# Kernel tuning notes

Hardware: AMD Instinct MI355X
Metric: run time of the kernel (lower is better)

The kernel has to match this reference:

```python
import jax, jax.numpy as jnp
import numpy as np

N_USER = 100000
N_ITEM = 50000
EMB = 64
LAYERS = 3
N_INTER = 2000000
BATCH = 4096


def setup_inputs() -> dict:
    key = jax.random.key(0)
    ks = jax.random.split(key, 12)
    N = N_USER + N_ITEM
    # bipartite interactions u -> i, symmetrized
    u = jax.random.randint(ks[0], (N_INTER,), 0, N_USER, dtype=jnp.int32)
    i = jax.random.randint(ks[1], (N_INTER,), 0, N_ITEM, dtype=jnp.int32) + N_USER
    edge_src = jnp.concatenate([u, i])
    edge_dst = jnp.concatenate([i, u])
    # symmetric normalization D^-1/2 A D^-1/2 (as in getSparseGraph)
    deg = jnp.bincount(edge_dst, length=N).astype(jnp.float32)
    d_inv_sqrt = jnp.where(deg > 0, jax.lax.rsqrt(jnp.maximum(deg, 1.0)), 0.0)
    edge_w = d_inv_sqrt[edge_src] * d_inv_sqrt[edge_dst]
    s = 1.0 / np.sqrt(EMB)  # xavier-ish scale
    inp = {
        "user_emb": jax.random.normal(ks[2], (N_USER, EMB), jnp.float32) * s,
        "item_emb": jax.random.normal(ks[3], (N_ITEM, EMB), jnp.float32) * s,
        "W_gc": jax.random.normal(ks[4], (LAYERS, EMB, EMB), jnp.float32) * s,
        "b_gc": jax.random.normal(ks[5], (LAYERS, 1, EMB), jnp.float32) * s,
        "W_bi": jax.random.normal(ks[6], (LAYERS, EMB, EMB), jnp.float32) * s,
        "b_bi": jax.random.normal(ks[7], (LAYERS, 1, EMB), jnp.float32) * s,
        "edge_w": edge_w,
        "edge_src": edge_src,
        "edge_dst": edge_dst,
        "users": jax.random.randint(ks[8], (BATCH,), 0, N_USER, dtype=jnp.int64),
        "pos_items": jax.random.randint(ks[9], (BATCH,), 0, N_ITEM, dtype=jnp.int64),
        "neg_items": jax.random.randint(ks[10], (BATCH,), 0, N_ITEM, dtype=jnp.int64),
    }
    return inp


def reference(user_emb, item_emb, W_gc, b_gc, W_bi, b_bi, edge_w,
              edge_src, edge_dst, users, pos_items, neg_items):
    n_user = user_emb.shape[0]
    N = n_user + item_emb.shape[0]
    ego = jnp.concatenate([user_emb, item_emb], axis=0)  # [N, d]
    all_embeddings = [ego]
    for k in range(W_gc.shape[0]):
        # SpMM: side = A_hat @ ego  (gather + weighted scatter-add)
        side = jax.ops.segment_sum(ego[edge_src] * edge_w[:, None], edge_dst,
                                   num_segments=N)
        sum_e = side @ W_gc[k] + b_gc[k]
        bi_e = (ego * side) @ W_bi[k] + b_bi[k]
        ego = jax.nn.leaky_relu(sum_e + bi_e, negative_slope=0.2)
        # dropout omitted (eval mode / identity for deterministic baseline)
        nrm = jnp.linalg.norm(ego, axis=1, keepdims=True)
        all_embeddings.append(ego / jnp.maximum(nrm, 1e-12))
    all_e = jnp.concatenate(all_embeddings, axis=1)  # [N, (L+1)*d]
    u_g = all_e[:n_user][users]
    i_g = all_e[n_user:]
    return (u_g, i_g[pos_items], i_g[neg_items])
```

## Files before the change

### kernel.cpp

```cpp
#include <hip/hip_runtime.h>

#define EMB 64
#define B2SHIFT 8
#define B2ROWS 256
#define MAXB 1024

typedef short v8s __attribute__((ext_vector_type(8)));
typedef float v4f __attribute__((ext_vector_type(4)));

__device__ __forceinline__ float b2f(unsigned short u) {
    return __uint_as_float(((unsigned int)u) << 16);
}
__device__ __forceinline__ unsigned short f2b(float f) {
    unsigned int u = __float_as_uint(f);
    u += 0x7FFF + ((u >> 16) & 1);
    return (unsigned short)(u >> 16);
}

__global__ void k_init_ego(const float* __restrict__ user_emb,
                           const float* __restrict__ item_emb,
                           const float* __restrict__ dsq,
                           unsigned short* __restrict__ egob,
                           unsigned short* __restrict__ egow,
                           unsigned short* __restrict__ all_eb,
                           int n_user, int N) {
    int idx = blockIdx.x * blockDim.x + threadIdx.x;
    int total = N * EMB;
    if (idx >= total) return;
    int n = idx >> 6;
    int c = idx & 63;
    float v = (n < n_user) ? user_emb[idx] : item_emb[(size_t)(n - n_user) * EMB + c];
    unsigned short b = f2b(v);
    egob[idx] = b;
    egow[idx] = f2b(dsq[n] * v);
    all_eb[(size_t)n * 256 + c] = b;
}

__global__ __launch_bounds__(256) void k_bhist(const int* __restrict__ dst,
                                               int* __restrict__ bins,
                                               int M, int nb2) {
    __shared__ int h[MAXB];
    for (int i = threadIdx.x; i < nb2; i += 256) h[i] = 0;
    __syncthreads();
    for (int e = blockIdx.x * 256 + threadIdx.x; e < M; e += gridDim.x * 256)
        atomicAdd(&h[dst[e] >> B2SHIFT], 1);
    __syncthreads();
    for (int i = threadIdx.x; i < nb2; i += 256)
        if (h[i]) atomicAdd(&bins[i], h[i]);
}

__global__ __launch_bounds__(1024) void k_bscan(const int* __restrict__ bins,
                                                int* __restrict__ boff,
                                                int* __restrict__ bcur,
                                                int* __restrict__ row_ptr,
                                                int P, int N) {
    __shared__ int buf[1024];
    int tid = threadIdx.x;
    int v = (tid < P) ? bins[tid] : 0;
    buf[tid] = v;
    __syncthreads();
    for (int d = 1; d < 1024; d <<= 1) {
        int add = (tid >= d) ? buf[tid - d] : 0;
        __syncthreads();
        buf[tid] += add;
        __syncthreads();
    }
    if (tid < P) {
        int excl = buf[tid] - v;
        boff[tid] = excl;
        bcur[tid] = excl;
    }
    if (tid == P - 1) {
        boff[P] = buf[tid];
        row_ptr[N] = buf[tid];
    }
}

__global__ __launch_bounds__(256) void k_bin(const int* __restrict__ src,
                                             const int* __restrict__ dst,
                                             int* __restrict__ bcur,
                                             int* __restrict__ binned,
                                             int M, int nb2) {
    __shared__ int hist[MAXB];
    __shared__ int runcur[MAXB];
    int chunk = (M + gridDim.x - 1) / gridDim.x;
    int lo = blockIdx.x * chunk;
    int hi = min(lo + chunk, M);
    for (int i = threadIdx.x; i < nb2; i += 256) hist[i] = 0;
    __syncthreads();
    for (int e = lo + threadIdx.x; e < hi; e += 256)
        atomicAdd(&hist[dst[e] >> B2SHIFT], 1);
    __syncthreads();
    for (int i = threadIdx.x; i < nb2; i += 256) {
        int c = hist[i];
        runcur[i] = c ? atomicAdd(&bcur[i], c) : 0;
    }
    __syncthreads();
    for (int e = lo + threadIdx.x; e < hi; e += 256) {
        int d = dst[e];
        int pos = atomicAdd(&runcur[d >> B2SHIFT], 1);
        binned[pos] = (src[e] << B2SHIFT) | (d & (B2ROWS - 1));
    }
}

__global__ __launch_bounds__(256) void k_csrb(const int* __restrict__ boff,
                                              const int* __restrict__ binned,
                                              int* __restrict__ row_ptr,
                                              float* __restrict__ dsq,
                                              int* __restrict__ csr, int N) {
    __shared__ int hist[B2ROWS];
    __shared__ int scan[B2ROWS];
    int b = blockIdx.x;
    int beg = boff[b], end = boff[b + 1];
    int tid = threadIdx.x;
    hist[tid] = 0;
    __syncthreads();
    for (int e = beg + tid; e < end; e += 256)
        atomicAdd(&hist[binned[e] & (B2ROWS - 1)], 1);
    __syncthreads();
    int c = hist[tid];
    scan[tid] = c;
    __syncthreads();
    for (int d = 1; d < B2ROWS; d <<= 1) {
        int add = (tid >= d) ? scan[tid - d] : 0;
        __syncthreads();
        scan[tid] += add;
        __syncthreads();
    }
    int excl = beg + scan[tid] - c;
    int node = (b << B2SHIFT) + tid;
    if (node < N) {
        row_ptr[node] = excl;
        dsq[node] = (c > 0) ? rsqrtf((float)c) : 0.0f;
    }
    __syncthreads();
    hist[tid] = excl;
    __syncthreads();
    for (int e = beg + tid; e < end; e += 256) {
        int v = binned[e];
        int pos = atomicAdd(&hist[v & (B2ROWS - 1)], 1);
        csr[pos] = v >> B2SHIFT;
    }
}

__global__ __launch_bounds__(256) void k_side(const int* __restrict__ row_ptr,
                                              const int* __restrict__ csr,
                                              const float* __restrict__ dsq,
                                              const unsigned short* __restrict__ egow,
                                              const unsigned short* __restrict__ egob,
                                              unsigned short* __restrict__ X, int N) {
    int wave = threadIdx.x >> 6;
    int lane = threadIdx.x & 63;
    int n = blockIdx.x * 4 + wave;
    if (n >= N) return;
    int beg = __builtin_amdgcn_readfirstlane(row_ptr[n]);
    int end = __builtin_amdgcn_readfirstlane(row_ptr[n + 1]);
    float a0 = 0.f, a1 = 0.f, a2 = 0.f, a3 = 0.f;
    int e = beg;
    while (e < end) {
        int take = end - e;
        if (take > 64) take = 64;
        int vidx = csr[min(e + lane, end - 1)];
        int j = 0;
        for (; j + 8 <= take; j += 8) {
            int s0 = __builtin_amdgcn_readlane(vidx, j + 0);
            int s1 = __builtin_amdgcn_readlane(vidx, j + 1);
            int s2 = __builtin_amdgcn_readlane(vidx, j + 2);
            int s3 = __builtin_amdgcn_readlane(vidx, j + 3);
            int s4 = __builtin_amdgcn_readlane(vidx, j + 4);
            int s5 = __builtin_amdgcn_readlane(vidx, j + 5);
            int s6 = __builtin_amdgcn_readlane(vidx, j + 6);
            int s7 = __builtin_amdgcn_readlane(vidx, j + 7);
            float v0 = b2f(egow[(size_t)s0 * EMB + lane]);
            float v1 = b2f(egow[(size_t)s1 * EMB + lane]);
            float v2 = b2f(egow[(size_t)s2 * EMB + lane]);
            float v3 = b2f(egow[(size_t)s3 * EMB + lane]);
            float v4 = b2f(egow[(size_t)s4 * EMB + lane]);
            float v5 = b2f(egow[(size_t)s5 * EMB + lane]);
            float v6 = b2f(egow[(size_t)s6 * EMB + lane]);
            float v7 = b2f(egow[(size_t)s7 * EMB + lane]);
            a0 += v0 + v4;
            a1 += v1 + v5;
            a2 += v2 + v6;
            a3 += v3 + v7;
        }
        for (; j < take; j++) {
            int s = __builtin_amdgcn_readlane(vidx, j);
            a0 += b2f(egow[(size_t)s * EMB + lane]);
        }
        e += take;
    }
    float s = dsq[n] * ((a0 + a1) + (a2 + a3));
    float eg = b2f(egob[(size_t)n * EMB + lane]);
    X[(size_t)n * 128 + lane] = f2b(s);
    X[(size_t)n * 128 + 64 + lane] = f2b(s * eg);
}

__global__ __launch_bounds__(256, 2) void k_mt(
        const unsigned short* __restrict__ X,
        unsigned short* __restrict__ egob, unsigned short* __restrict__ egow,
        const float* __restrict__ dsq,
        const float* __restrict__ Wgc, const float* __restrict__ bgc,
        const float* __restrict__ Wbi, const float* __restrict__ bbi,
        unsigned short* __restrict__ all_eb, int N, int layer_col) {
    __shared__ unsigned short sWT[64 * 136];
    __shared__ float sB[64];
    int tid = threadIdx.x;
    for (int i = tid; i < 64 * 64; i += 256) {
        int k = i >> 6, n = i & 63;
        sWT[n * 136 + k]      = f2b(Wgc[i]);
        sWT[n * 136 + 64 + k] = f2b(Wbi[i]);
    }
    if (tid < 64) sB[tid] = bgc[tid] + bbi[tid];
    __syncthreads();

    int wave = tid >> 6, lane = tid & 63;
    int q = lane >> 4, col = lane & 15;

    v8s Bf[4][4];
#pragma unroll
    for (int nt = 0; nt < 4; nt++)
#pragma unroll
        for (int kt = 0; kt < 4; kt++)
            Bf[nt][kt] = *(const v8s*)&sWT[(nt * 16 + col) * 136 + kt * 32 + q * 8];

    int nrt = (N + 15) >> 4;
    int rt0 = (blockIdx.x * 4 + wave) * 4;
    int rt1 = min(rt0 + 4, nrt);
    for (int t = rt0; t < rt1; t++) {
        int r0 = t << 4;
        int rowA = min(r0 + col, N - 1);
        v8s Af[4];
#pragma unroll
        for (int kt = 0; kt < 4; kt++)
            Af[kt] = *(const v8s*)&X[(size_t)rowA * 128 + kt * 32 + q * 8];
        v4f acc[4];
#pragma unroll
        for (int nt = 0; nt < 4; nt++) {
            float b = sB[nt * 16 + col];
            acc[nt] = (v4f){b, b, b, b};
        }
#pragma unroll
        for (int kt = 0; kt < 4; kt++)
#pragma unroll
            for (int nt = 0; nt < 4; nt++)
                acc[nt] = __builtin_amdgcn_mfma_f32_16x16x32_bf16(
                    Af[kt], Bf[nt][kt], acc[nt], 0, 0, 0);
#pragma unroll
        for (int reg = 0; reg < 4; reg++) {
            int row = r0 + q * 4 + reg;
            float v[4];
            float ssq = 0.f;
#pragma unroll
            for (int nt = 0; nt < 4; nt++) {
                float x = acc[nt][reg];
                x = x > 0.f ? x : 0.2f * x;
                v[nt] = x;
                ssq += x * x;
            }
            ssq += __shfl_xor(ssq, 1, 64);
            ssq += __shfl_xor(ssq, 2, 64);
            ssq += __shfl_xor(ssq, 4, 64);
            ssq += __shfl_xor(ssq, 8, 64);
            float inv = 1.0f / fmaxf(sqrtf(ssq), 1e-12f);
            if (row < N) {
                float dn = dsq[row];
#pragma unroll
                for (int nt = 0; nt < 4; nt++) {
                    int c = nt * 16 + col;
                    egob[(size_t)row * EMB + c] = f2b(v[nt]);
                    egow[(size_t)row * EMB + c] = f2b(v[nt] * dn);
                    all_eb[(size_t)row * 256 + layer_col + c] = f2b(v[nt] * inv);
                }
            }
        }
    }
}

__global__ void k_gather(const unsigned short* __restrict__ all_eb,
                         const int* __restrict__ users,
                         const int* __restrict__ pos,
                         const int* __restrict__ neg,
                         float* __restrict__ out, int n_user, int batch) {
    int idx = blockIdx.x * blockDim.x + threadIdx.x;
    int total = batch * 256;
    if (idx >= 3 * total) return;
    int which = idx / total;
    int r = idx - which * total;
    int b = r >> 8;
    int c = r & 255;
    int node;
    if (which == 0) node = users[b];
    else if (which == 1) node = n_user + pos[b];
    else node = n_user + neg[b];
    out[idx] = b2f(all_eb[(size_t)node * 256 + c]);
}

static inline size_t align256(size_t x) { return (x + 255) & ~(size_t)255; }

extern "C" void kernel_launch(void* const* d_in, const int* in_sizes, int n_in,
                              void* d_out, int out_size, void* d_ws, size_t ws_size,
                              hipStream_t stream) {
    const float* user_emb = (const float*)d_in[0];
    const float* item_emb = (const float*)d_in[1];
    const float* W_gc = (const float*)d_in[2];
    const float* b_gc = (const float*)d_in[3];
    const float* W_bi = (const float*)d_in[4];
    const float* b_bi = (const float*)d_in[5];
    const int* edge_src = (const int*)d_in[7];
    const int* edge_dst = (const int*)d_in[8];
    const int* users = (const int*)d_in[9];
    const int* pos = (const int*)d_in[10];
    const int* neg = (const int*)d_in[11];

    int n_user = in_sizes[0] / EMB;
    int n_item = in_sizes[1] / EMB;
    int N = n_user + n_item;
    int M = in_sizes[6];
    int layers = in_sizes[2] / (EMB * EMB);
    int batch = in_sizes[9];
    float* out = (float*)d_out;

    int nb2 = (N + B2ROWS - 1) >> B2SHIFT;
    int nrt = (N + 15) >> 4;

    char* p = (char*)d_ws;
    unsigned short* egob = (unsigned short*)p;   p += align256((size_t)N * EMB * 2);
    unsigned short* egow = (unsigned short*)p;   p += align256((size_t)N * EMB * 2);
    unsigned short* X = (unsigned short*)p;      p += align256((size_t)N * 128 * 2);
    unsigned short* all_eb = (unsigned short*)p; p += align256((size_t)N * 256 * 2);
    float* dsq = (float*)p;            p += align256((size_t)N * 4);
    int* row_ptr = (int*)p;            p += align256((size_t)(N + 1) * 4);
    int* bins = (int*)p;               p += align256((size_t)nb2 * 4);
    int* boff = (int*)p;               p += align256((size_t)(nb2 + 1) * 4);
    int* bcur = (int*)p;               p += align256((size_t)nb2 * 4);
    int* binned = (int*)p;             p += align256((size_t)M * 4);
    int* csr = (int*)p;                p += align256((size_t)M * 4);

    hipMemsetAsync(bins, 0, (size_t)nb2 * 4, stream);

    k_bhist<<<512, 256, 0, stream>>>(edge_dst, bins, M, nb2);
    k_bscan<<<1, 1024, 0, stream>>>(bins, boff, bcur, row_ptr, nb2, N);
    k_bin<<<512, 256, 0, stream>>>(edge_src, edge_dst, bcur, binned, M, nb2);
    k_csrb<<<nb2, 256, 0, stream>>>(boff, binned, row_ptr, dsq, csr, N);

    k_init_ego<<<(N * EMB + 255) / 256, 256, 0, stream>>>(
        user_emb, item_emb, dsq, egob, egow, all_eb, n_user, N);

    for (int k = 0; k < layers; k++) {
        k_side<<<(N + 3) / 4, 256, 0, stream>>>(row_ptr, csr, dsq, egow, egob, X, N);
        k_mt<<<(nrt + 15) / 16, 256, 0, stream>>>(
            X, egob, egow, dsq,
            W_gc + (size_t)k * EMB * EMB, b_gc + (size_t)k * EMB,
            W_bi + (size_t)k * EMB * EMB, b_bi + (size_t)k * EMB,
            all_eb, N, (k + 1) * EMB);
    }

    k_gather<<<(3 * batch * 256 + 255) / 256, 256, 0, stream>>>(
        all_eb, users, pos, neg, out, n_user, batch);
}
```

Measured before the change: 622.3 us.

## Fuse ego init into CSR build, unroll gather by 16, nontemporal all_eb stores

Folds the initial embedding conversion (bf16 ego, degree-scaled ego, layer-0 output) into the per-bin CSR build kernel, so one launch and the re-read of dsq go away. Adds a 16-wide unrolled neighbour gather loop in the SpMM kernel to keep more loads in flight. Writes to the concatenated output buffer use nontemporal stores so they pollute the cache less. The unrolled loop raises register pressure, and the fused kernel does serial work inside 586 blocks, which may lower parallelism for the init step.

```diff
diff --git a/kernel.cpp b/kernel.cpp
--- a/kernel.cpp
+++ b/kernel.cpp
@@ -15,25 +15,6 @@
     unsigned int u = __float_as_uint(f);
     u += 0x7FFF + ((u >> 16) & 1);
     return (unsigned short)(u >> 16);
-}
-
-__global__ void k_init_ego(const float* __restrict__ user_emb,
-                           const float* __restrict__ item_emb,
-                           const float* __restrict__ dsq,
-                           unsigned short* __restrict__ egob,
-                           unsigned short* __restrict__ egow,
-                           unsigned short* __restrict__ all_eb,
-                           int n_user, int N) {
-    int idx = blockIdx.x * blockDim.x + threadIdx.x;
-    int total = N * EMB;
-    if (idx >= total) return;
-    int n = idx >> 6;
-    int c = idx & 63;
-    float v = (n < n_user) ? user_emb[idx] : item_emb[(size_t)(n - n_user) * EMB + c];
-    unsigned short b = f2b(v);
-    egob[idx] = b;
-    egow[idx] = f2b(dsq[n] * v);
-    all_eb[(size_t)n * 256 + c] = b;
 }
 
 __global__ __launch_bounds__(256) void k_bhist(const int* __restrict__ dst,
@@ -103,13 +84,17 @@
     }
 }
 
-__global__ __launch_bounds__(256) void k_csrb(const int* __restrict__ boff,
-                                              const int* __restrict__ binned,
-                                              int* __restrict__ row_ptr,
-                                              float* __restrict__ dsq,
-                                              int* __restrict__ csr, int N) {
+__global__ __launch_bounds__(256) void k_csrb(
+        const int* __restrict__ boff, const int* __restrict__ binned,
+        int* __restrict__ row_ptr, float* __restrict__ dsq,
+        int* __restrict__ csr,
+        const float* __restrict__ user_emb, const float* __restrict__ item_emb,
+        unsigned short* __restrict__ egob, unsigned short* __restrict__ egow,
+        unsigned short* __restrict__ all_eb,
+        int n_user, int N) {
     __shared__ int hist[B2ROWS];
     __shared__ int scan[B2ROWS];
+    __shared__ float sdsq[B2ROWS];
     int b = blockIdx.x;
     int beg = boff[b], end = boff[b + 1];
     int tid = threadIdx.x;
@@ -129,10 +114,12 @@
     }
     int excl = beg + scan[tid] - c;
     int node = (b << B2SHIFT) + tid;
+    float dv = (c > 0) ? rsqrtf((float)c) : 0.0f;
     if (node < N) {
         row_ptr[node] = excl;
-        dsq[node] = (c > 0) ? rsqrtf((float)c) : 0.0f;
-    }
+        dsq[node] = dv;
+    }
+    sdsq[tid] = dv;
     __syncthreads();
     hist[tid] = excl;
     __syncthreads();
@@ -140,6 +127,18 @@
         int v = binned[e];
         int pos = atomicAdd(&hist[v & (B2ROWS - 1)], 1);
         csr[pos] = v >> B2SHIFT;
+    }
+    int node0 = b << B2SHIFT;
+    int nn = min(B2ROWS, N - node0);
+    for (int i = tid; i < nn * EMB; i += 256) {
+        int ln = i >> 6, c2 = i & 63;
+        int n2 = node0 + ln;
+        float v = (n2 < n_user) ? user_emb[(size_t)n2 * EMB + c2]
+                                : item_emb[(size_t)(n2 - n_user) * EMB + c2];
+        unsigned short bb = f2b(v);
+        egob[(size_t)n2 * EMB + c2] = bb;
+        egow[(size_t)n2 * EMB + c2] = f2b(sdsq[ln] * v);
+        __builtin_nontemporal_store(bb, &all_eb[(size_t)n2 * 256 + c2]);
     }
 }
 
@@ -162,6 +161,23 @@
         if (take > 64) take = 64;
         int vidx = csr[min(e + lane, end - 1)];
         int j = 0;
+        for (; j + 16 <= take; j += 16) {
+            int s[16];
+#pragma unroll
+            for (int u = 0; u < 16; u++)
+                s[u] = __builtin_amdgcn_readlane(vidx, j + u);
+            float v[16];
+#pragma unroll
+            for (int u = 0; u < 16; u++)
+                v[u] = b2f(egow[(size_t)s[u] * EMB + lane]);
+#pragma unroll
+            for (int u = 0; u < 16; u += 4) {
+                a0 += v[u + 0];
+                a1 += v[u + 1];
+                a2 += v[u + 2];
+                a3 += v[u + 3];
+            }
+        }
         for (; j + 8 <= take; j += 8) {
             int s0 = __builtin_amdgcn_readlane(vidx, j + 0);
             int s1 = __builtin_amdgcn_readlane(vidx, j + 1);
@@ -270,7 +286,9 @@
                     int c = nt * 16 + col;
                     egob[(size_t)row * EMB + c] = f2b(v[nt]);
                     egow[(size_t)row * EMB + c] = f2b(v[nt] * dn);
-                    all_eb[(size_t)row * 256 + layer_col + c] = f2b(v[nt] * inv);
+                    __builtin_nontemporal_store(
+                        f2b(v[nt] * inv),
+                        &all_eb[(size_t)row * 256 + layer_col + c]);
                 }
             }
         }
@@ -342,10 +360,9 @@
     k_bhist<<<512, 256, 0, stream>>>(edge_dst, bins, M, nb2);
     k_bscan<<<1, 1024, 0, stream>>>(bins, boff, bcur, row_ptr, nb2, N);
     k_bin<<<512, 256, 0, stream>>>(edge_src, edge_dst, bcur, binned, M, nb2);
-    k_csrb<<<nb2, 256, 0, stream>>>(boff, binned, row_ptr, dsq, csr, N);
-
-    k_init_ego<<<(N * EMB + 255) / 256, 256, 0, stream>>>(
-        user_emb, item_emb, dsq, egob, egow, all_eb, n_user, N);
+    k_csrb<<<nb2, 256, 0, stream>>>(boff, binned, row_ptr, dsq, csr,
+                                    user_emb, item_emb, egob, egow, all_eb,
+                                    n_user, N);
 
     for (int k = 0; k < layers; k++) {
         k_side<<<(N + 3) / 4, 256, 0, stream>>>(row_ptr, csr, dsq, egow, egob, X, N);
```

After: 635.2 us. +2.1%, slower.
